# Optimization experiments

Measured on AMD Instinct MI355X. Metric: run time of the kernel, lower is better.

The kernel has to match this reference:

```python
import jax, jax.numpy as jnp
import numpy as np

C_SIZE = 512
STRIDE = 4
OUT = C_SIZE // STRIDE          # 128, density grid side
GRID = OUT * OUT                # 16384
REG = 10.0
ITERS = 100                     # num_of_iter_in_ot
M_EPS = 1e-16
B = 8                           # batch of images
N = 1024                        # points per image (fixed for jit; ragged in torch)


def setup_inputs() -> dict:
    key = jax.random.key(0)
    k1, k2 = jax.random.split(key, 2)
    d = jax.random.uniform(k1, (B, 1, OUT, OUT), dtype=jnp.float32)
    # normed_density sums to 1 per image (a probability map), unnormed is raw density
    normed_density = d / jnp.sum(d, axis=(1, 2, 3), keepdims=True)
    unnormed_density = d * 100.0
    points = jax.random.uniform(k2, (B, N, 2), dtype=jnp.float32) * C_SIZE
    gt_discrete = jnp.zeros((B, 1, OUT, OUT), dtype=jnp.float32)
    return {"normed_density": normed_density, "unnormed_density": unnormed_density,
            "points": points, "gt_discrete": gt_discrete}


def _per_image(nd, und, pts):
    # nd, und: (1, OUT, OUT); pts: (N, 2)
    cood = jnp.arange(0, C_SIZE, STRIDE, dtype=jnp.float32) + STRIDE / 2.0  # (OUT,)
    x = pts[:, 0:1]
    y = pts[:, 1:2]
    # squared-distance decomposition: -2*x*c + x^2 + c^2
    x_dis = x * x - 2.0 * x * cood[None, :] + cood[None, :] ** 2  # (N, OUT)
    y_dis = y * y - 2.0 * y * cood[None, :] + cood[None, :] ** 2  # (N, OUT)
    dis = (y_dis[:, :, None] + x_dis[:, None, :]).reshape(N, GRID)  # (N, GRID)

    a = jnp.full((N,), 1.0 / N, dtype=jnp.float32)          # target_prob (points)
    b = jax.lax.stop_gradient(nd.reshape(-1))               # source_prob (density, detached)
    K = jnp.exp(-dis / REG)                                 # (N, GRID) Gibbs kernel

    def step(carry, _):
        u, v = carry
        v = b / (u @ K + M_EPS)      # K^T u
        u = a / (K @ v + M_EPS)
        return (u, v), None

    u0 = jnp.full((N,), 1.0 / N, dtype=jnp.float32)
    v0 = jnp.full((GRID,), 1.0 / GRID, dtype=jnp.float32)
    (u, v), _ = jax.lax.scan(step, (u0, v0), None, length=ITERS)

    P = u[:, None] * K * v[None, :]                          # transport plan (N, GRID)
    beta = jax.lax.stop_gradient(REG * jnp.log(v + M_EPS))   # source dual potential

    ot_obj = jnp.sum(nd.reshape(-1) * beta)
    sd = jax.lax.stop_gradient(und.reshape(-1))              # source_density (detached)
    sc = sd.sum()
    denom = sc * sc + 1e-8
    im_grad = (sc / denom) * beta - (sd * beta).sum() / denom  # detached in torch
    loss = jnp.sum(und.reshape(-1) * im_grad)
    wd = jax.lax.stop_gradient(jnp.sum(dis * P))              # .item() in torch
    return loss, wd, ot_obj


def reference(normed_density, unnormed_density, points, gt_discrete):
    losses, wds, ots = jax.vmap(_per_image)(normed_density, unnormed_density, points)
    # torch returns (loss, wd, ot_obj_values); packed as a (3,) array here
    return jnp.stack([losses.sum(), wds.sum(), ots.sum()])
```

## Files before the change

### kernel.cpp

```cpp
#include <hip/hip_runtime.h>


#define N_IMG   8
#define N_PTS   1024
#define OUT_D   128
#define N_CELLS (OUT_D * OUT_D)
#define WIN     11
#define RT      5
#define WINX    18
#define N_TILE  1024
#define N_CHUNK 16
#define CAPE    32768
#define EPS     1e-16f
#define INV_N   (1.0f / 1024.0f)
#define N_ITERS 100

typedef unsigned int   uint_t;
typedef unsigned short u16;
typedef float v2f __attribute__((ext_vector_type(2)));

__device__ __forceinline__ u16 f2bf(float f) {
    uint_t b = __float_as_uint(f);
    b += 0x7FFFu + ((b >> 16) & 1u);
    return (u16)(b >> 16);
}
__device__ __forceinline__ float bf2f(u16 h)   { return __uint_as_float(((uint_t)h) << 16); }
__device__ __forceinline__ float bflo(uint_t w){ return __uint_as_float(w << 16); }
__device__ __forceinline__ float bfhi(uint_t w){ return __uint_as_float(w & 0xFFFF0000u); }
__device__ __forceinline__ uint_t cvt_pk_bf16(float lo, float hi) {
    uint_t r;
    asm volatile("v_cvt_pk_bf16_f32 %0, %1, %2" : "=v"(r) : "v"(lo), "v"(hi));
    return r;
}
__device__ __forceinline__ float dot2bf(uint_t a, uint_t b, float c) {
    float r;
    asm volatile("v_dot2_f32_bf16 %0, %1, %2, %3" : "=v"(r) : "v"(a), "v"(b), "v"(c));
    return r;
}

__global__ __launch_bounds__(1024) void ot_build(
    const float* __restrict__ pts, uint4* __restrict__ cstream,
    u16* __restrict__ pstream, u16* __restrict__ tileofg,
    uint_t* __restrict__ cbaseg, uint_t* __restrict__ cleng)
{
    __shared__ uint_t chist[N_CELLS];
    __shared__ u16    P[128 * 129];
    __shared__ u16    c0tab[N_PTS];
    __shared__ u16    tslot[N_TILE];
    __shared__ u16    tlen[N_TILE];
    __shared__ u16    tof[N_TILE];
    __shared__ uint_t bins[1025];
    __shared__ uint_t cbase_l[N_CHUNK + 1];

    const int img = blockIdx.x, tid = threadIdx.x;
    for (int i = tid; i < N_CELLS; i += 1024) chist[i] = 0;
    for (int i = tid; i < 1025;    i += 1024) bins[i] = 0;
    __syncthreads();

    const float x = pts[(img * N_PTS + tid) * 2 + 0];
    const float y = pts[(img * N_PTS + tid) * 2 + 1];
    const int nx = (int)floorf((x - 2.f) * 0.25f + 0.5f);
    const int ny = (int)floorf((y - 2.f) * 0.25f + 0.5f);
    const int ix0 = min(max(nx - RT, 0), OUT_D - WIN);
    const int iy0 = min(max(ny - RT, 0), OUT_D - WIN);
    const float xx = x * x, yy = y * y;
    float kx[WIN], ky[WIN];
#pragma unroll
    for (int k = 0; k < WIN; ++k) {
        float cx = (float)(4 * (ix0 + k) + 2);
        kx[k] = __expf(-((xx - 2.f * x * cx) + cx * cx) * 0.1f);
        float cy = (float)(4 * (iy0 + k) + 2);
        ky[k] = __expf(-((yy - 2.f * y * cy) + cy * cy) * 0.1f);
    }
    const int cell0 = (iy0 << 7) | ix0;
    c0tab[tid] = (u16)cell0;
    atomicAdd(&chist[cell0], 1u);
    __syncthreads();

    if (tid < 128) {
        uint_t acc = 0;
        P[tid * 129 + 0] = 0;
        for (int c = 0; c < 128; ++c) { acc += chist[(tid << 7) + c]; P[tid * 129 + c + 1] = (u16)acc; }
    }
    __syncthreads();

    int rank = 0;
    for (int p = 0; p < N_PTS; ++p) rank += (p < tid && c0tab[p] == (u16)cell0) ? 1 : 0;

    {
        int ty = tid >> 5, tx = tid & 31;
        int rlo = max(4 * ty - 10, 0), rhi = min(4 * ty + 3, OUT_D - WIN);
        int xlo = max(4 * tx - 10, 0), xhi = min(4 * tx + 3, OUT_D - WIN);
        uint_t len = 0;
        for (int r = rlo; r <= rhi; ++r)
            len += (uint_t)P[r * 129 + xhi + 1] - (uint_t)P[r * 129 + xlo];
        tlen[tid] = (u16)len;
        atomicAdd(&bins[len], 1u);
    }
    __syncthreads();
    if (tid == 0) {
        uint_t acc = 0;
        for (int L = 1024; L >= 0; --L) { uint_t t = bins[L]; bins[L] = acc; acc += t; }
    }
    __syncthreads();
    {
        uint_t slot = atomicAdd(&bins[tlen[tid]], 1u);
        tslot[tid] = (u16)slot;
        tof[slot] = (u16)tid;
    }
    __syncthreads();
    if (tid < N_CHUNK) cbase_l[tid] = tlen[tof[tid * 64]];
    __syncthreads();
    if (tid == 0) {
        uint_t acc = 0;
        for (int c = 0; c < N_CHUNK; ++c) { uint_t l = cbase_l[c]; cbase_l[c] = acc; acc += l * 64u; }
        cbase_l[N_CHUNK] = acc;
    }
    __syncthreads();
    tileofg[img * N_TILE + tid] = tof[tid];
    if (tid < N_CHUNK) {
        cbaseg[img * N_CHUNK + tid] = cbase_l[tid];
        cleng[img * N_CHUNK + tid]  = tlen[tof[tid * 64]];
    }

    uint4* cs = cstream + (size_t)img * CAPE;
    u16*   ps = pstream + (size_t)img * CAPE;
    const int tya = iy0 >> 2, tyb = (iy0 + 10) >> 2;
    const int txa = ix0 >> 2, txb = (ix0 + 10) >> 2;
    for (int ty = tya; ty <= tyb; ++ty) {
        for (int tx = txa; tx <= txb; ++tx) {
            int ti = (ty << 5) | tx;
            int slot = tslot[ti];
            int xlo = max(4 * tx - 10, 0), xhi = min(4 * tx + 3, OUT_D - WIN);
            int rlo = max(4 * ty - 10, 0);
            uint_t idx = (uint_t)rank + (uint_t)P[iy0 * 129 + ix0] - (uint_t)P[iy0 * 129 + xlo];
            for (int r = rlo; r < iy0; ++r)
                idx += (uint_t)P[r * 129 + xhi + 1] - (uint_t)P[r * 129 + xlo];
            uint_t eofs = cbase_l[slot >> 6] + idx * 64u + (uint_t)(slot & 63);
            if (eofs < CAPE) {
                u16 kxp[4], kyp[4];
#pragma unroll
                for (int c = 0; c < 4; ++c) {
                    int dk = 4 * tx + c - ix0;
                    kxp[c] = ((unsigned)dk < 11u) ? f2bf(kx[dk]) : (u16)0;
                    int dj = 4 * ty + c - iy0;
                    kyp[c] = ((unsigned)dj < 11u) ? f2bf(ky[dj]) : (u16)0;
                }
                cs[eofs] = make_uint4((uint_t)kxp[0] | ((uint_t)kxp[1] << 16),
                                      (uint_t)kxp[2] | ((uint_t)kxp[3] << 16),
                                      (uint_t)kyp[0] | ((uint_t)kyp[1] << 16),
                                      (uint_t)kyp[2] | ((uint_t)kyp[3] << 16));
                ps[eofs] = (u16)tid;
            }
        }
    }
}

__device__ __forceinline__ float blk_sum(float v, volatile float* red)
{
#pragma unroll
    for (int o = 32; o; o >>= 1) v += __shfl_xor(v, o, 64);
    int wave = threadIdx.x >> 6, lane = threadIdx.x & 63;
    if (lane == 0) red[wave] = v;
    __syncthreads();
    if (threadIdx.x < 64) {
        float t = (lane < 16) ? red[lane] : 0.0f;
#pragma unroll
        for (int o = 8; o; o >>= 1) t += __shfl_xor(t, o, 64);
        if (lane == 0) red[0] = t;
    }
    __syncthreads();
    float r = red[0];
    __syncthreads();
    return r;
}

__global__ __launch_bounds__(1024) void ot_fused(
    const float* __restrict__ nd, const float* __restrict__ und,
    const float* __restrict__ pts, const uint4* __restrict__ cstream,
    const u16* __restrict__ pstream, const u16* __restrict__ tileofg,
    const uint_t* __restrict__ cbaseg, const uint_t* __restrict__ cleng,
    float* __restrict__ parts)
{
    __shared__ __align__(16) u16 Vh[N_CELLS + 32];
    __shared__ float  su[N_PTS];
    __shared__ u16    bktab[N_PTS];
    __shared__ u16    sorted_pt[N_PTS];
    __shared__ u16    leftover[N_PTS];
    __shared__ uint_t ng[8];
    __shared__ uint_t og[8];
    __shared__ uint_t cbase_l[N_CHUNK];
    __shared__ uint_t clen_l[N_CHUNK];
    __shared__ float  red[64];

    const int img = blockIdx.x, tid = threadIdx.x;
    const int w = tid >> 6, lane = tid & 63;
    const float* ndi = nd + img * N_CELLS;

    if (tid < N_CHUNK) { cbase_l[tid] = cbaseg[img * N_CHUNK + tid]; clen_l[tid] = cleng[img * N_CHUNK + tid]; }
    if (tid < 32) Vh[N_CELLS + tid] = 0;
    if (tid < 8)  ng[tid] = 0;
    su[tid] = INV_N;
    __syncthreads();

    {
        float x_ = pts[(img * N_PTS + tid) * 2 + 0];
        int nx_ = (int)floorf((x_ - 2.f) * 0.25f + 0.5f);
        int i0_ = min(max(nx_ - RT, 0), OUT_D - WIN);
        bktab[tid] = (u16)(((i0_ & ~7) >> 3) & 7);
    }
    __syncthreads();
    {
        const int g = (int)bktab[tid];
        int rnk = 0;
        for (int p = 0; p < tid; ++p) rnk += ((int)bktab[p] == g) ? 1 : 0;
        atomicAdd(&ng[g], 1u);
        __syncthreads();
        if (tid == 0) {
            uint_t acc = 0;
            for (int b = 0; b < 8; ++b) { og[b] = acc; acc += (ng[b] > 128u) ? ng[b] - 128u : 0u; }
        }
        __syncthreads();
        if (rnk < 128) sorted_pt[rnk * 8 + g] = (u16)tid;
        else           leftover[og[g] + (uint_t)(rnk - 128)] = (u16)tid;
        __syncthreads();
        const int c = tid >> 3, j = tid & 7;
        if (c >= (int)ng[j]) {
            int E = 0;
#pragma unroll
            for (int j2 = 0; j2 < 8; ++j2) {
                int nj = (int)ng[j2];
                E += max(0, c - nj) + ((j2 < j && c >= nj) ? 1 : 0);
            }
            sorted_pt[tid] = leftover[E];
        }
    }
    __syncthreads();
    const int pp = (int)sorted_pt[tid];

    const int tile = (int)tileofg[img * N_TILE + w * 64 + lane];
    const int ty4 = (tile >> 5) * 4, tx4 = (tile & 31) * 4;
    float4 b4[4];
#pragma unroll
    for (int r = 0; r < 4; ++r) b4[r] = *(const float4*)(ndi + (ty4 + r) * OUT_D + tx4);
    const uint4* csb = cstream + (size_t)img * CAPE + cbase_l[w] + lane;
    const u16*   psb = pstream + (size_t)img * CAPE + cbase_l[w] + lane;
    const int    alen = (int)clen_l[w];

    const float x = pts[(img * N_PTS + pp) * 2 + 0];
    const float y = pts[(img * N_PTS + pp) * 2 + 1];
    const int nx = (int)floorf((x - 2.f) * 0.25f + 0.5f);
    const int ny = (int)floorf((y - 2.f) * 0.25f + 0.5f);
    const int ix0 = min(max(nx - RT, 0), OUT_D - WIN);
    const int iy0 = min(max(ny - RT, 0), OUT_D - WIN);
    const int ixq = ix0 & ~7;
    const float xx = x * x, yy = y * y;
    uint_t kxp[WINX / 2];
    float  kyr[WIN];
#pragma unroll
    for (int q = 0; q < WINX / 2; ++q) {
        float kv[2];
#pragma unroll
        for (int h = 0; h < 2; ++h) {
            int col = ixq + 2 * q + h, dk = col - ix0;
            float cx = (float)(4 * col + 2);
            kv[h] = ((unsigned)dk < 11u) ? __expf(-((xx - 2.f * x * cx) + cx * cx) * 0.1f) : 0.f;
        }
        kxp[q] = cvt_pk_bf16(kv[0], kv[1]);
    }
#pragma unroll
    for (int j = 0; j < WIN; ++j) {
        float cy = (float)(4 * (iy0 + j) + 2);
        kyr[j] = __expf(-((yy - 2.f * y * cy) + cy * cy) * 0.1f);
    }
    float ureg = INV_N;
    const u16* vbp = &Vh[iy0 * OUT_D + ixq];

    for (int it = 0; it < N_ITERS; ++it) {
        v2f acc2[8] = {};
        uint4 cw = make_uint4(0u, 0u, 0u, 0u); u16 pid = 0;
        if (alen > 0) { cw = csb[0]; pid = psb[0]; }
        for (int t = 1; t <= alen; ++t) {
            uint4 cwn = csb[(size_t)t * 64];
            u16   pn  = psb[(size_t)t * 64];
            float uv = su[pid & 1023u];
            v2f kxa = {bflo(cw.x), bfhi(cw.x)};
            v2f kxb = {bflo(cw.y), bfhi(cw.y)};
            float u0 = uv * bflo(cw.z), u1 = uv * bfhi(cw.z);
            float u2 = uv * bflo(cw.w), u3 = uv * bfhi(cw.w);
            v2f s0 = {u0, u0}, s1 = {u1, u1}, s2 = {u2, u2}, s3 = {u3, u3};
            acc2[0] += s0 * kxa;  acc2[1] += s0 * kxb;
            acc2[2] += s1 * kxa;  acc2[3] += s1 * kxb;
            acc2[4] += s2 * kxa;  acc2[5] += s2 * kxb;
            acc2[6] += s3 * kxa;  acc2[7] += s3 * kxb;
            cw = cwn; pid = pn;
        }
#pragma unroll
        for (int r = 0; r < 4; ++r) {
            float v0 = b4[r].x * __builtin_amdgcn_rcpf(acc2[2 * r][0] + EPS);
            float v1 = b4[r].y * __builtin_amdgcn_rcpf(acc2[2 * r][1] + EPS);
            float v2 = b4[r].z * __builtin_amdgcn_rcpf(acc2[2 * r + 1][0] + EPS);
            float v3 = b4[r].w * __builtin_amdgcn_rcpf(acc2[2 * r + 1][1] + EPS);
            uint2 wv = make_uint2(cvt_pk_bf16(v0, v1), cvt_pk_bf16(v2, v3));
            *(uint2*)&Vh[(ty4 + r) * OUT_D + tx4] = wv;
        }
        __syncthreads();

        float tt = 0.f;
#pragma unroll
        for (int j = 0; j < WIN; ++j) {
            const u16* row = vbp + j * OUT_D;
            uint4 w0 = *(const uint4*)(row);
            uint4 w1 = *(const uint4*)(row + 8);
            uint_t w2 = *(const uint_t*)(row + 16);
            float rs0, rs1;
            rs0 = dot2bf(kxp[0], w0.x, 0.f);
            rs1 = dot2bf(kxp[1], w0.y, 0.f);
            rs0 = dot2bf(kxp[2], w0.z, rs0);
            rs1 = dot2bf(kxp[3], w0.w, rs1);
            rs0 = dot2bf(kxp[4], w1.x, rs0);
            rs1 = dot2bf(kxp[5], w1.y, rs1);
            rs0 = dot2bf(kxp[6], w1.z, rs0);
            rs1 = dot2bf(kxp[7], w1.w, rs1);
            rs0 = dot2bf(kxp[8], w2,   rs0);
            tt = fmaf(kyr[j], rs0 + rs1, tt);
        }
        ureg = INV_N / (tt + EPS);
        su[pp] = ureg;
        __syncthreads();
    }

    const float* sdi = und + img * N_CELLS;
    float sc = 0.f, T = 0.f, ot = 0.f;
#pragma unroll
    for (int r = 0; r < 16; ++r) {
        int c = r * 1024 + tid;
        float beta = 10.0f * logf(bf2f(Vh[c]) + EPS);
        float s = sdi[c];
        sc += s;
        T  = fmaf(s, beta, T);
        ot = fmaf(ndi[c], beta, ot);
    }
    sc = blk_sum(sc, red);
    T  = blk_sum(T,  red);
    ot = blk_sum(ot, red);
    float denom = sc * sc + 1e-8f;
    float c1 = sc / denom, c2 = T / denom;

    float loss = 0.f;
#pragma unroll
    for (int r = 0; r < 16; ++r) {
        int c = r * 1024 + tid;
        float beta = 10.0f * logf(bf2f(Vh[c]) + EPS);
        loss = fmaf(sdi[c], fmaf(c1, beta, -c2), loss);
    }
    loss = blk_sum(loss, red);

    float wd = 0.f;
#pragma unroll
    for (int j = 0; j < WIN; ++j) {
        float cy = (float)(4 * (iy0 + j) + 2);
        float dy = (yy - 2.f * y * cy) + cy * cy;
        const u16* row = vbp + j * OUT_D;
        float skv = 0.f, sdkv = 0.f;
#pragma unroll
        for (int d = 0; d < WINX; ++d) {
            int col = ixq + d, dk = col - ix0;
            float cx = (float)(4 * col + 2);
            float kxv = ((unsigned)dk < 11u) ? __expf(-((xx - 2.f * x * cx) + cx * cx) * 0.1f) : 0.f;
            float dx = (xx - 2.f * x * cx) + cx * cx;
            float kv = kxv * bf2f(row[d]);
            skv += kv;
            sdkv = fmaf(dx, kv, sdkv);
        }
        wd = fmaf(kyr[j], fmaf(dy, skv, sdkv), wd);
    }
    wd *= ureg;
    wd = blk_sum(wd, red);

    if (tid == 0) {
        parts[img * 3 + 0] = loss;
        parts[img * 3 + 1] = wd;
        parts[img * 3 + 2] = ot;
    }
}

__global__ void ot_sum(const float* __restrict__ parts, float* __restrict__ out)
{
    int t = threadIdx.x;
    if (t < 3) {
        float s = 0.f;
        for (int i = 0; i < N_IMG; ++i) s += parts[i * 3 + t];
        out[t] = s;
    }
}

extern "C" void kernel_launch(void* const* d_in, const int* in_sizes, int n_in,
                              void* d_out, int out_size, void* d_ws, size_t ws_size,
                              hipStream_t stream_)
{
    const float* nd  = (const float*)d_in[0];
    const float* und = (const float*)d_in[1];
    const float* pts = (const float*)d_in[2];

    char* ws = (char*)d_ws;
    uint4*  cstream = (uint4*)ws;
    u16*    pstream = (u16*)(ws + 4194304);
    u16*    tileofg = (u16*)(ws + 4718592);
    uint_t* cbaseg  = (uint_t*)(ws + 4734976);
    uint_t* cleng   = (uint_t*)(ws + 4735488);
    float*  parts   = (float*)(ws + 4736000);

    hipMemsetAsync(cstream, 0, 4194304, stream_);
    ot_build<<<N_IMG, 1024, 0, stream_>>>(pts, cstream, pstream, tileofg, cbaseg, cleng);
    ot_fused<<<N_IMG, 1024, 0, stream_>>>(nd, und, pts, cstream, pstream, tileofg,
                                          cbaseg, cleng, parts);
    ot_sum<<<1, 64, 0, stream_>>>(parts, (float*)d_out);
}
```

Measured before the change: 703.3 us.

## Split each image's Sinkhorn loop across two cooperating blocks with global barriers

The fused Sinkhorn kernel now launches two blocks per image. Each block computes half of the grid-cell tiles (with each tile's entry stream split across the two half-waves and combined by a shuffle) and half of the points. The two blocks exchange the v and u vectors through global memory using relaxed atomics and a spin-wait pair barrier after each half-iteration. The aim is to use twice as many compute units for the latency-bound iteration loop, in exchange for two inter-block global barriers and global round trips per iteration. Correctness also depends on both blocks of a pair being resident at the same time.

Result: slower. 939.4 us (+33.6%).

```diff
diff --git a/kernel.cpp b/kernel.cpp
--- a/kernel.cpp
+++ b/kernel.cpp
@@ -1,22 +1,24 @@
 #include <hip/hip_runtime.h>
 
 
-#define N_IMG   8
-#define N_PTS   1024
-#define OUT_D   128
-#define N_CELLS (OUT_D * OUT_D)
-#define WIN     11
-#define RT      5
-#define WINX    18
-#define N_TILE  1024
-#define N_CHUNK 16
-#define CAPE    32768
-#define EPS     1e-16f
-#define INV_N   (1.0f / 1024.0f)
-#define N_ITERS 100
-
-typedef unsigned int   uint_t;
-typedef unsigned short u16;
+#define N_IMG    8
+#define N_PTS    1024
+#define HALF_PTS 512
+#define OUT_D    128
+#define N_CELLS  (OUT_D * OUT_D)
+#define WIN      11
+#define RT       5
+#define WINX     18
+#define N_TILE   1024
+#define N_CHUNK  32
+#define CAPE     32768
+#define EPS      1e-16f
+#define INV_N    (1.0f / 1024.0f)
+#define N_ITERS  100
+
+typedef unsigned int       uint_t;
+typedef unsigned short     u16;
+typedef unsigned long long u64;
 typedef float v2f __attribute__((ext_vector_type(2)));
 
 __device__ __forceinline__ u16 f2bf(float f) {
@@ -36,6 +38,19 @@
     float r;
     asm volatile("v_dot2_f32_bf16 %0, %1, %2, %3" : "=v"(r) : "v"(a), "v"(b), "v"(c));
     return r;
+}
+__device__ __forceinline__ void  gst64(u64* p, u64 v)   { __hip_atomic_store(p, v, __ATOMIC_RELAXED, __HIP_MEMORY_SCOPE_AGENT); }
+__device__ __forceinline__ u64   gld64(const u64* p)    { return __hip_atomic_load(p, __ATOMIC_RELAXED, __HIP_MEMORY_SCOPE_AGENT); }
+__device__ __forceinline__ void  gstf(float* p, float v){ __hip_atomic_store(p, v, __ATOMIC_RELAXED, __HIP_MEMORY_SCOPE_AGENT); }
+__device__ __forceinline__ float gldf(const float* p)   { return __hip_atomic_load(p, __ATOMIC_RELAXED, __HIP_MEMORY_SCOPE_AGENT); }
+
+__device__ __forceinline__ void pair_barrier(uint_t* ctr, uint_t target) {
+    if (threadIdx.x == 0) {
+        __hip_atomic_fetch_add(ctr, 1u, __ATOMIC_RELEASE, __HIP_MEMORY_SCOPE_AGENT);
+        while (__hip_atomic_load(ctr, __ATOMIC_ACQUIRE, __HIP_MEMORY_SCOPE_AGENT) < target)
+            __builtin_amdgcn_s_sleep(2);
+    }
+    __syncthreads();
 }
 
 __global__ __launch_bounds__(1024) void ot_build(
@@ -109,18 +124,18 @@
         tof[slot] = (u16)tid;
     }
     __syncthreads();
-    if (tid < N_CHUNK) cbase_l[tid] = tlen[tof[tid * 64]];
+    if (tid < N_CHUNK) cbase_l[tid] = ((uint_t)tlen[tof[tid * 32]] + 1u) & ~1u;
     __syncthreads();
     if (tid == 0) {
         uint_t acc = 0;
-        for (int c = 0; c < N_CHUNK; ++c) { uint_t l = cbase_l[c]; cbase_l[c] = acc; acc += l * 64u; }
+        for (int c = 0; c < N_CHUNK; ++c) { uint_t l = cbase_l[c]; cbase_l[c] = acc; acc += l * 32u; }
         cbase_l[N_CHUNK] = acc;
     }
     __syncthreads();
     tileofg[img * N_TILE + tid] = tof[tid];
     if (tid < N_CHUNK) {
         cbaseg[img * N_CHUNK + tid] = cbase_l[tid];
-        cleng[img * N_CHUNK + tid]  = tlen[tof[tid * 64]];
+        cleng[img * N_CHUNK + tid]  = ((uint_t)tlen[tof[tid * 32]] + 1u) & ~1u;
     }
 
     uint4* cs = cstream + (size_t)img * CAPE;
@@ -136,7 +151,7 @@
             uint_t idx = (uint_t)rank + (uint_t)P[iy0 * 129 + ix0] - (uint_t)P[iy0 * 129 + xlo];
             for (int r = rlo; r < iy0; ++r)
                 idx += (uint_t)P[r * 129 + xhi + 1] - (uint_t)P[r * 129 + xlo];
-            uint_t eofs = cbase_l[slot >> 6] + idx * 64u + (uint_t)(slot & 63);
+            uint_t eofs = cbase_l[slot >> 5] + idx * 32u + (uint_t)(slot & 31);
             if (eofs < CAPE) {
                 u16 kxp[4], kyp[4];
 #pragma unroll
@@ -180,22 +195,24 @@
     const float* __restrict__ pts, const uint4* __restrict__ cstream,
     const u16* __restrict__ pstream, const u16* __restrict__ tileofg,
     const uint_t* __restrict__ cbaseg, const uint_t* __restrict__ cleng,
-    float* __restrict__ parts)
+    u16* __restrict__ Vg, float* __restrict__ sug,
+    float* __restrict__ partsL, float* __restrict__ partsO,
+    float* __restrict__ partsW, uint_t* __restrict__ bars)
 {
     __shared__ __align__(16) u16 Vh[N_CELLS + 32];
     __shared__ float  su[N_PTS];
-    __shared__ u16    bktab[N_PTS];
-    __shared__ u16    sorted_pt[N_PTS];
-    __shared__ u16    leftover[N_PTS];
-    __shared__ uint_t ng[8];
-    __shared__ uint_t og[8];
-    __shared__ uint_t cbase_l[N_CHUNK];
-    __shared__ uint_t clen_l[N_CHUNK];
+    __shared__ u16    bktab[HALF_PTS];
+    __shared__ u16    sorted_pt[HALF_PTS];
+    __shared__ u16    leftover[HALF_PTS];
+    __shared__ uint_t ng[8], og[8];
+    __shared__ uint_t cbase_l[N_CHUNK], clen_l[N_CHUNK];
     __shared__ float  red[64];
 
-    const int img = blockIdx.x, tid = threadIdx.x;
-    const int w = tid >> 6, lane = tid & 63;
+    const int img = blockIdx.x >> 1, half = blockIdx.x & 1;
+    const int tid = threadIdx.x, w = tid >> 6, lane = tid & 63;
     const float* ndi = nd + img * N_CELLS;
+    uint_t* barA = &bars[img * 32 + 0];
+    uint_t* barB = &bars[img * 32 + 1];
 
     if (tid < N_CHUNK) { cbase_l[tid] = cbaseg[img * N_CHUNK + tid]; clen_l[tid] = cleng[img * N_CHUNK + tid]; }
     if (tid < 32) Vh[N_CELLS + tid] = 0;
@@ -203,27 +220,32 @@
     su[tid] = INV_N;
     __syncthreads();
 
-    {
-        float x_ = pts[(img * N_PTS + tid) * 2 + 0];
+    int g_ = 0, rnk = 0;
+    if (tid < HALF_PTS) {
+        int gp = img * N_PTS + half * HALF_PTS + tid;
+        float x_ = pts[gp * 2 + 0];
         int nx_ = (int)floorf((x_ - 2.f) * 0.25f + 0.5f);
         int i0_ = min(max(nx_ - RT, 0), OUT_D - WIN);
         bktab[tid] = (u16)(((i0_ & ~7) >> 3) & 7);
     }
     __syncthreads();
-    {
-        const int g = (int)bktab[tid];
-        int rnk = 0;
-        for (int p = 0; p < tid; ++p) rnk += ((int)bktab[p] == g) ? 1 : 0;
-        atomicAdd(&ng[g], 1u);
-        __syncthreads();
-        if (tid == 0) {
-            uint_t acc = 0;
-            for (int b = 0; b < 8; ++b) { og[b] = acc; acc += (ng[b] > 128u) ? ng[b] - 128u : 0u; }
-        }
-        __syncthreads();
-        if (rnk < 128) sorted_pt[rnk * 8 + g] = (u16)tid;
-        else           leftover[og[g] + (uint_t)(rnk - 128)] = (u16)tid;
-        __syncthreads();
+    if (tid < HALF_PTS) {
+        g_ = (int)bktab[tid];
+        for (int p = 0; p < tid; ++p) rnk += ((int)bktab[p] == g_) ? 1 : 0;
+        atomicAdd(&ng[g_], 1u);
+    }
+    __syncthreads();
+    if (tid == 0) {
+        uint_t acc = 0;
+        for (int b = 0; b < 8; ++b) { og[b] = acc; acc += (ng[b] > 64u) ? ng[b] - 64u : 0u; }
+    }
+    __syncthreads();
+    if (tid < HALF_PTS) {
+        if (rnk < 64) sorted_pt[rnk * 8 + g_] = (u16)tid;
+        else          leftover[og[g_] + (uint_t)(rnk - 64)] = (u16)tid;
+    }
+    __syncthreads();
+    if (tid < HALF_PTS) {
         const int c = tid >> 3, j = tid & 7;
         if (c >= (int)ng[j]) {
             int E = 0;
@@ -236,19 +258,22 @@
         }
     }
     __syncthreads();
-    const int pp = (int)sorted_pt[tid];
-
-    const int tile = (int)tileofg[img * N_TILE + w * 64 + lane];
+    const int gp2 = img * N_PTS + half * HALF_PTS + ((tid < HALF_PTS) ? (int)sorted_pt[tid] : 0);
+
+    const int cidx = 2 * w + half;
+    const int slot = cidx * 32 + (lane & 31);
+    const int tile = (int)tileofg[img * N_TILE + slot];
     const int ty4 = (tile >> 5) * 4, tx4 = (tile & 31) * 4;
     float4 b4[4];
 #pragma unroll
     for (int r = 0; r < 4; ++r) b4[r] = *(const float4*)(ndi + (ty4 + r) * OUT_D + tx4);
-    const uint4* csb = cstream + (size_t)img * CAPE + cbase_l[w] + lane;
-    const u16*   psb = pstream + (size_t)img * CAPE + cbase_l[w] + lane;
-    const int    alen = (int)clen_l[w];
-
-    const float x = pts[(img * N_PTS + pp) * 2 + 0];
-    const float y = pts[(img * N_PTS + pp) * 2 + 1];
+    const uint4* csb = cstream + (size_t)img * CAPE + cbase_l[cidx] + (lane & 31);
+    const u16*   psb = pstream + (size_t)img * CAPE + cbase_l[cidx] + (lane & 31);
+    const int    alen = (int)clen_l[cidx];
+    const int    tstart = (lane >= 32) ? 1 : 0;
+
+    const float x = pts[gp2 * 2 + 0];
+    const float y = pts[gp2 * 2 + 1];
     const int nx = (int)floorf((x - 2.f) * 0.25f + 0.5f);
     const int ny = (int)floorf((y - 2.f) * 0.25f + 0.5f);
     const int ix0 = min(max(nx - RT, 0), OUT_D - WIN);
@@ -275,14 +300,17 @@
     }
     float ureg = INV_N;
     const u16* vbp = &Vh[iy0 * OUT_D + ixq];
+    u64* Vg64 = (u64*)(Vg + img * N_CELLS);
 
     for (int it = 0; it < N_ITERS; ++it) {
         v2f acc2[8] = {};
         uint4 cw = make_uint4(0u, 0u, 0u, 0u); u16 pid = 0;
-        if (alen > 0) { cw = csb[0]; pid = psb[0]; }
-        for (int t = 1; t <= alen; ++t) {
-            uint4 cwn = csb[(size_t)t * 64];
-            u16   pn  = psb[(size_t)t * 64];
+        if (alen > 0) { cw = csb[(size_t)tstart * 32]; pid = psb[(size_t)tstart * 32]; }
+        const int hn = alen >> 1;
+        for (int i = 1; i <= hn; ++i) {
+            int t = 2 * i + tstart;
+            uint4 cwn = csb[(size_t)t * 32];
+            u16   pn  = psb[(size_t)t * 32];
             float uv = su[pid & 1023u];
             v2f kxa = {bflo(cw.x), bfhi(cw.x)};
             v2f kxb = {bflo(cw.y), bfhi(cw.y)};
@@ -296,103 +324,121 @@
             cw = cwn; pid = pn;
         }
 #pragma unroll
-        for (int r = 0; r < 4; ++r) {
-            float v0 = b4[r].x * __builtin_amdgcn_rcpf(acc2[2 * r][0] + EPS);
-            float v1 = b4[r].y * __builtin_amdgcn_rcpf(acc2[2 * r][1] + EPS);
-            float v2 = b4[r].z * __builtin_amdgcn_rcpf(acc2[2 * r + 1][0] + EPS);
-            float v3 = b4[r].w * __builtin_amdgcn_rcpf(acc2[2 * r + 1][1] + EPS);
-            uint2 wv = make_uint2(cvt_pk_bf16(v0, v1), cvt_pk_bf16(v2, v3));
-            *(uint2*)&Vh[(ty4 + r) * OUT_D + tx4] = wv;
+        for (int r = 0; r < 8; ++r) {
+            acc2[r][0] += __shfl_xor(acc2[r][0], 32);
+            acc2[r][1] += __shfl_xor(acc2[r][1], 32);
+        }
+        if (lane < 32) {
+#pragma unroll
+            for (int r = 0; r < 4; ++r) {
+                float v0 = b4[r].x * __builtin_amdgcn_rcpf(acc2[2 * r][0] + EPS);
+                float v1 = b4[r].y * __builtin_amdgcn_rcpf(acc2[2 * r][1] + EPS);
+                float v2 = b4[r].z * __builtin_amdgcn_rcpf(acc2[2 * r + 1][0] + EPS);
+                float v3 = b4[r].w * __builtin_amdgcn_rcpf(acc2[2 * r + 1][1] + EPS);
+                u64 pk = (u64)cvt_pk_bf16(v0, v1) | ((u64)cvt_pk_bf16(v2, v3) << 32);
+                gst64(&Vg64[((ty4 + r) * OUT_D + tx4) >> 2], pk);
+            }
         }
         __syncthreads();
-
-        float tt = 0.f;
+        pair_barrier(barA, 2u * (uint_t)(it + 1));
+        {
+            u64* dst = (u64*)Vh;
+            const u64* src = (const u64*)Vg64;
+#pragma unroll
+            for (int r = 0; r < 4; ++r) dst[r * 1024 + tid] = gld64(&src[r * 1024 + tid]);
+        }
+        __syncthreads();
+
+        if (tid < HALF_PTS) {
+            float tt = 0.f;
+#pragma unroll
+            for (int j = 0; j < WIN; ++j) {
+                const u16* row = vbp + j * OUT_D;
+                uint4 w0 = *(const uint4*)(row);
+                uint4 w1 = *(const uint4*)(row + 8);
+                uint_t w2 = *(const uint_t*)(row + 16);
+                float rs0, rs1;
+                rs0 = dot2bf(kxp[0], w0.x, 0.f);
+                rs1 = dot2bf(kxp[1], w0.y, 0.f);
+                rs0 = dot2bf(kxp[2], w0.z, rs0);
+                rs1 = dot2bf(kxp[3], w0.w, rs1);
+                rs0 = dot2bf(kxp[4], w1.x, rs0);
+                rs1 = dot2bf(kxp[5], w1.y, rs1);
+                rs0 = dot2bf(kxp[6], w1.z, rs0);
+                rs1 = dot2bf(kxp[7], w1.w, rs1);
+                rs0 = dot2bf(kxp[8], w2,   rs0);
+                tt = fmaf(kyr[j], rs0 + rs1, tt);
+            }
+            ureg = INV_N / (tt + EPS);
+            gstf(&sug[gp2], ureg);
+        }
+        __syncthreads();
+        pair_barrier(barB, 2u * (uint_t)(it + 1));
+        su[tid] = gldf(&sug[img * N_PTS + tid]);
+        __syncthreads();
+    }
+
+    const float* sdi = und + img * N_CELLS;
+    if (half == 0) {
+        float sc = 0.f, T = 0.f, ot = 0.f;
+#pragma unroll
+        for (int r = 0; r < 16; ++r) {
+            int c = r * 1024 + tid;
+            float beta = 10.0f * logf(bf2f(Vh[c]) + EPS);
+            float s = sdi[c];
+            sc += s;
+            T  = fmaf(s, beta, T);
+            ot = fmaf(ndi[c], beta, ot);
+        }
+        sc = blk_sum(sc, red);
+        T  = blk_sum(T,  red);
+        ot = blk_sum(ot, red);
+        float denom = sc * sc + 1e-8f;
+        float c1 = sc / denom, c2 = T / denom;
+        float loss = 0.f;
+#pragma unroll
+        for (int r = 0; r < 16; ++r) {
+            int c = r * 1024 + tid;
+            float beta = 10.0f * logf(bf2f(Vh[c]) + EPS);
+            loss = fmaf(sdi[c], fmaf(c1, beta, -c2), loss);
+        }
+        loss = blk_sum(loss, red);
+        if (tid == 0) { partsL[img] = loss; partsO[img] = ot; }
+    }
+
+    float wd = 0.f;
+    if (tid < HALF_PTS) {
 #pragma unroll
         for (int j = 0; j < WIN; ++j) {
+            float cy = (float)(4 * (iy0 + j) + 2);
+            float dy = (yy - 2.f * y * cy) + cy * cy;
             const u16* row = vbp + j * OUT_D;
-            uint4 w0 = *(const uint4*)(row);
-            uint4 w1 = *(const uint4*)(row + 8);
-            uint_t w2 = *(const uint_t*)(row + 16);
-            float rs0, rs1;
-            rs0 = dot2bf(kxp[0], w0.x, 0.f);
-            rs1 = dot2bf(kxp[1], w0.y, 0.f);
-            rs0 = dot2bf(kxp[2], w0.z, rs0);
-            rs1 = dot2bf(kxp[3], w0.w, rs1);
-            rs0 = dot2bf(kxp[4], w1.x, rs0);
-            rs1 = dot2bf(kxp[5], w1.y, rs1);
-            rs0 = dot2bf(kxp[6], w1.z, rs0);
-            rs1 = dot2bf(kxp[7], w1.w, rs1);
-            rs0 = dot2bf(kxp[8], w2,   rs0);
-            tt = fmaf(kyr[j], rs0 + rs1, tt);
-        }
-        ureg = INV_N / (tt + EPS);
-        su[pp] = ureg;
-        __syncthreads();
-    }
-
-    const float* sdi = und + img * N_CELLS;
-    float sc = 0.f, T = 0.f, ot = 0.f;
-#pragma unroll
-    for (int r = 0; r < 16; ++r) {
-        int c = r * 1024 + tid;
-        float beta = 10.0f * logf(bf2f(Vh[c]) + EPS);
-        float s = sdi[c];
-        sc += s;
-        T  = fmaf(s, beta, T);
-        ot = fmaf(ndi[c], beta, ot);
-    }
-    sc = blk_sum(sc, red);
-    T  = blk_sum(T,  red);
-    ot = blk_sum(ot, red);
-    float denom = sc * sc + 1e-8f;
-    float c1 = sc / denom, c2 = T / denom;
-
-    float loss = 0.f;
-#pragma unroll
-    for (int r = 0; r < 16; ++r) {
-        int c = r * 1024 + tid;
-        float beta = 10.0f * logf(bf2f(Vh[c]) + EPS);
-        loss = fmaf(sdi[c], fmaf(c1, beta, -c2), loss);
-    }
-    loss = blk_sum(loss, red);
-
-    float wd = 0.f;
-#pragma unroll
-    for (int j = 0; j < WIN; ++j) {
-        float cy = (float)(4 * (iy0 + j) + 2);
-        float dy = (yy - 2.f * y * cy) + cy * cy;
-        const u16* row = vbp + j * OUT_D;
-        float skv = 0.f, sdkv = 0.f;
-#pragma unroll
-        for (int d = 0; d < WINX; ++d) {
-            int col = ixq + d, dk = col - ix0;
-            float cx = (float)(4 * col + 2);
-            float kxv = ((unsigned)dk < 11u) ? __expf(-((xx - 2.f * x * cx) + cx * cx) * 0.1f) : 0.f;
-            float dx = (xx - 2.f * x * cx) + cx * cx;
-            float kv = kxv * bf2f(row[d]);
-            skv += kv;
-            sdkv = fmaf(dx, kv, sdkv);
-        }
-        wd = fmaf(kyr[j], fmaf(dy, skv, sdkv), wd);
-    }
-    wd *= ureg;
+            float skv = 0.f, sdkv = 0.f;
+#pragma unroll
+            for (int d = 0; d < WINX; ++d) {
+                int col = ixq + d, dk = col - ix0;
+                float cx = (float)(4 * col + 2);
+                float kxv = ((unsigned)dk < 11u) ? __expf(-((xx - 2.f * x * cx) + cx * cx) * 0.1f) : 0.f;
+                float dx = (xx - 2.f * x * cx) + cx * cx;
+                float kv = kxv * bf2f(row[d]);
+                skv += kv;
+                sdkv = fmaf(dx, kv, sdkv);
+            }
+            wd = fmaf(kyr[j], fmaf(dy, skv, sdkv), wd);
+        }
+        wd *= ureg;
+    }
     wd = blk_sum(wd, red);
-
-    if (tid == 0) {
-        parts[img * 3 + 0] = loss;
-        parts[img * 3 + 1] = wd;
-        parts[img * 3 + 2] = ot;
-    }
-}
-
-__global__ void ot_sum(const float* __restrict__ parts, float* __restrict__ out)
+    if (tid == 0) partsW[img * 2 + half] = wd;
+}
+
+__global__ void ot_sum(const float* __restrict__ pl, const float* __restrict__ po,
+                       const float* __restrict__ pw, float* __restrict__ out)
 {
     int t = threadIdx.x;
-    if (t < 3) {
-        float s = 0.f;
-        for (int i = 0; i < N_IMG; ++i) s += parts[i * 3 + t];
-        out[t] = s;
-    }
+    if (t == 0) { float s = 0.f; for (int i = 0; i < 8;  ++i) s += pl[i]; out[0] = s; }
+    if (t == 1) { float s = 0.f; for (int i = 0; i < 16; ++i) s += pw[i]; out[1] = s; }
+    if (t == 2) { float s = 0.f; for (int i = 0; i < 8;  ++i) s += po[i]; out[2] = s; }
 }
 
 extern "C" void kernel_launch(void* const* d_in, const int* in_sizes, int n_in,
@@ -408,12 +454,19 @@
     u16*    pstream = (u16*)(ws + 4194304);
     u16*    tileofg = (u16*)(ws + 4718592);
     uint_t* cbaseg  = (uint_t*)(ws + 4734976);
-    uint_t* cleng   = (uint_t*)(ws + 4735488);
-    float*  parts   = (float*)(ws + 4736000);
+    uint_t* cleng   = (uint_t*)(ws + 4736000);
+    u16*    Vg      = (u16*)(ws + 4737024);
+    float*  sug     = (float*)(ws + 4999168);
+    float*  partsL  = (float*)(ws + 5031936);
+    float*  partsO  = (float*)(ws + 5031968);
+    float*  partsW  = (float*)(ws + 5032000);
+    uint_t* bars    = (uint_t*)(ws + 5032064);
 
     hipMemsetAsync(cstream, 0, 4194304, stream_);
+    hipMemsetAsync(bars, 0, 1024, stream_);
     ot_build<<<N_IMG, 1024, 0, stream_>>>(pts, cstream, pstream, tileofg, cbaseg, cleng);
-    ot_fused<<<N_IMG, 1024, 0, stream_>>>(nd, und, pts, cstream, pstream, tileofg,
-                                          cbaseg, cleng, parts);
-    ot_sum<<<1, 64, 0, stream_>>>(parts, (float*)d_out);
-}
+    ot_fused<<<N_IMG * 2, 1024, 0, stream_>>>(nd, und, pts, cstream, pstream, tileofg,
+                                              cbaseg, cleng, Vg, sug,
+                                              partsL, partsO, partsW, bars);
+    ot_sum<<<1, 64, 0, stream_>>>(partsL, partsO, partsW, (float*)d_out);
+}
```
